# Kernel optimization log

Hardware: AMD Instinct MI355X
Metric: run time of the kernel (lower is better)

## Reference

```python
import jax, jax.numpy as jnp
import numpy as np

T, B, V, L = 512, 32, 512, 128
NEG = -1e9  # safe -inf surrogate (keeps logaddexp gradients finite)


def setup_inputs() -> dict:
    key = jax.random.key(0)
    k1, k2, k3 = jax.random.split(key, 3)
    log_probs = jax.nn.log_softmax(
        jax.random.normal(k1, (T, B, V), dtype=jnp.float32), axis=-1)
    # ASG transition parameter (init ones in the module; use small noise for a
    # non-degenerate reference). transition[i, j] = score of j -> i.
    transition = 0.1 * jax.random.normal(k2, (V, V), dtype=jnp.float32)
    targets = jax.random.randint(k3, (B, L), 0, V)
    input_lengths = jnp.full((B,), T, dtype=jnp.int32)
    target_lengths = jnp.full((B,), L, dtype=jnp.int32)
    return {"log_probs": log_probs, "transition": transition,
            "targets": targets, "input_lengths": input_lengths,
            "target_lengths": target_lengths}


def _fcc(log_probs, transition, input_lengths):
    """Fully-connected criterion: log-partition over all label paths. [B]"""
    def step(alpha, lp_t):  # alpha, lp_t: [B, V]
        # alpha'[b, i] = lp_t[b, i] + logsumexp_j(alpha[b, j] + trans[i, j])
        alpha = lp_t + jax.nn.logsumexp(
            alpha[:, None, :] + transition[None, :, :], axis=2)
        return alpha, jax.nn.logsumexp(alpha, axis=1)

    a0 = log_probs[0]
    _, tail = jax.lax.scan(step, a0, log_probs[1:])
    scores = jnp.concatenate(
        [jax.nn.logsumexp(a0, axis=1)[None], tail], axis=0)  # [T, B]
    return scores[input_lengths - 1, jnp.arange(scores.shape[1])]


def _fac(log_probs, transition, targets, input_lengths, target_lengths):
    """Forced-alignment criterion: DP constrained to the target label seq. [B]"""
    Tt, Bb, _ = log_probs.shape
    Ll = targets.shape[1]
    trans_self = transition[targets, targets]                    # [B, L] stay
    trans_prev = transition[targets[:, 1:], targets[:, :-1]]     # [B, L-1] advance
    # emit[t, b, s] = log_probs[t, b, targets[b, s]]
    emit = jnp.take_along_axis(
        log_probs, jnp.broadcast_to(targets[None], (Tt, Bb, Ll)), axis=2)

    sel = (target_lengths - 1)[:, None]  # [B, 1]

    def final_of(beta):
        return jnp.take_along_axis(beta, sel, axis=1)[:, 0]

    beta0 = jnp.where(jnp.arange(Ll)[None, :] == 0, emit[0], NEG)  # [B, L]

    def step(beta, em_t):
        stay = beta + trans_self
        move = jnp.concatenate(
            [jnp.full((Bb, 1), NEG, beta.dtype),
             beta[:, :-1] + trans_prev], axis=1)
        beta = em_t + jnp.logaddexp(stay, move)
        return beta, final_of(beta)

    _, tail = jax.lax.scan(step, beta0, emit[1:])
    fins = jnp.concatenate([final_of(beta0)[None], tail], axis=0)  # [T, B]
    return fins[input_lengths - 1, jnp.arange(Bb)]


def reference(log_probs, transition, targets, input_lengths, target_lengths):
    # ASG loss (reduction='none'): FCC - FAC, shape [B]
    fcc = _fcc(log_probs, transition, input_lengths)
    fac = _fac(log_probs, transition, targets, input_lengths, target_lengths)
    return fcc - fac
```

## Files before the change

kernel.cpp:

```cpp
#include <hip/hip_runtime.h>
#include <stdint.h>

#define T_ 512
#define B_ 32
#define V_ 512
#define L_ 128
#define NEGF (-1000000000.0f)

#define SE_Q 69.0f
#define SU_Q 127.0f
#define LOGC 9.078313f

typedef int v4i __attribute__((ext_vector_type(4)));

template <int CTRL>
__device__ __forceinline__ int dppmov(int old_, int src) {
    return __builtin_amdgcn_update_dpp(old_, src, CTRL, 0xF, 0xF, false);
}
__device__ __forceinline__ float wave_max64(float x) {
    int xi = __float_as_int(x);
    x = fmaxf(x, __int_as_float(dppmov<0x111>(xi, xi))); xi = __float_as_int(x);
    x = fmaxf(x, __int_as_float(dppmov<0x112>(xi, xi))); xi = __float_as_int(x);
    x = fmaxf(x, __int_as_float(dppmov<0x114>(xi, xi))); xi = __float_as_int(x);
    x = fmaxf(x, __int_as_float(dppmov<0x118>(xi, xi))); xi = __float_as_int(x);
    x = fmaxf(x, __int_as_float(dppmov<0x142>(xi, xi))); xi = __float_as_int(x);
    x = fmaxf(x, __int_as_float(dppmov<0x143>(xi, xi)));
    return x;
}
__device__ __forceinline__ float wave_sum64(float x) {
    int xi = __float_as_int(x);
    x = x + __int_as_float(dppmov<0x111>(xi, xi)); xi = __float_as_int(x);
    x = x + __int_as_float(dppmov<0x112>(xi, xi)); xi = __float_as_int(x);
    x = x + __int_as_float(dppmov<0x114>(xi, xi)); xi = __float_as_int(x);
    x = x + __int_as_float(dppmov<0x118>(xi, xi)); xi = __float_as_int(x);
    x = x + __int_as_float(dppmov<0x142>(xi, xi)); xi = __float_as_int(x);
    x = x + __int_as_float(dppmov<0x143>(xi, xi));
    return x;
}
__device__ __forceinline__ unsigned fkey(float f) {
    unsigned u = __float_as_uint(f);
    return (u & 0x80000000u) ? ~u : (u | 0x80000000u);
}
__device__ __forceinline__ float funkey(unsigned k) {
    unsigned u = (k & 0x80000000u) ? (k ^ 0x80000000u) : ~k;
    return __uint_as_float(u);
}
__device__ __forceinline__ int sel4(v4i a, int r) {
    int x0 = (r & 1) ? a.y : a.x;
    int x1 = (r & 1) ? a.w : a.z;
    return (r & 2) ? x1 : x0;
}

__global__ void asg_prep(const float* __restrict__ trans, uint32_t* __restrict__ Et) {
    int o = blockIdx.x * blockDim.x + threadIdx.x;
    int d    = o & 3;
    int tid  = (o >> 2) & 511;
    int qreg = o >> 11;
    int tt = qreg >> 3, kt = qreg & 7;
    int w = tid >> 6, lane = tid & 63;
    int q = lane >> 4, n = lane & 15;
    int m  = 64 * w + 16 * tt + n;
    int k0 = 64 * kt + 16 * q + 4 * d;
    const float* tp = trans + (size_t)m * V_ + k0;
    uint32_t q0 = (uint32_t)fminf(127.0f, __expf(tp[0]) * SE_Q + 0.5f);
    uint32_t q1 = (uint32_t)fminf(127.0f, __expf(tp[1]) * SE_Q + 0.5f);
    uint32_t q2 = (uint32_t)fminf(127.0f, __expf(tp[2]) * SE_Q + 0.5f);
    uint32_t q3 = (uint32_t)fminf(127.0f, __expf(tp[3]) * SE_Q + 0.5f);
    Et[(size_t)o] = q0 | (q1 << 8) | (q2 << 16) | (q3 << 24);
}

__global__ __attribute__((amdgpu_flat_work_group_size(512, 512),
                          amdgpu_waves_per_eu(2, 2)))
void asg_main(
    const float* __restrict__ lp, const uint32_t* __restrict__ Et,
    const float* __restrict__ trans, const int* __restrict__ targets,
    const int* __restrict__ ilen, const int* __restrict__ tlen,
    float* __restrict__ fcc_ws, float* __restrict__ fac_ws)
{
    __shared__ float facb[256];
    __shared__ __align__(16) uint32_t u_lds[128];
    __shared__ unsigned mslot[2];
    __shared__ unsigned mslotE;
    __shared__ float sumf;

    const int bb  = blockIdx.x;
    const int tid = threadIdx.x;

    if (bb < B_) {
        const int b    = bb;
        const int lane = tid & 63;
        const int w    = tid >> 6;
        const int q    = lane >> 4;
        const int n    = lane & 15;
        const int tt_o = n >> 2;
        const int rg_o = n & 3;
        const int i    = 64 * w + 16 * tt_o + 4 * q + rg_o;
        const int Tlen = ilen[b];

        uint4 er4[32];
        {
            const uint4* Eq = (const uint4*)Et;
            #pragma unroll
            for (int t8 = 0; t8 < 32; ++t8) er4[t8] = Eq[t8 * 512 + tid];
        }

        float alpha = lp[(size_t)b * V_ + i];
        float lpv   = lp[(size_t)1 * (B_ * V_) + (size_t)b * V_ + i];
        if (tid == 511) { mslot[0] = 0u; mslot[1] = 0u; mslotE = 0u; sumf = 0.0f; }
        __syncthreads();

        for (int t = 1; t < Tlen; ++t) {
            {
                float mx = wave_max64(alpha);
                if (lane == 63) atomicMax(&mslot[(t - 1) & 1], fkey(mx));
            }
            __syncthreads();
            float m = funkey(mslot[(t - 1) & 1]);

            {
                float u = __expf(alpha - m);
                uint32_t qu = (uint32_t)(u * SU_Q + 0.5f);
                int pv = (int)(qu << (8 * (i & 3)));
                pv |= dppmov<0xB1>(pv, pv);
                pv |= dppmov<0x4E>(pv, pv);
                if ((i & 3) == 0) u_lds[i >> 2] = (uint32_t)pv;
            }
            if (tid == 511) mslot[t & 1] = 0u;
            __syncthreads();

            int tn = (t + 1 < Tlen) ? (t + 1) : t;
            float lpv_n = lp[(size_t)tn * (B_ * V_) + (size_t)b * V_ + i];

            uint4 bf[8];
            #pragma unroll
            for (int kt = 0; kt < 8; ++kt)
                bf[kt] = *(const uint4*)((const char*)u_lds + 64 * kt + 16 * q);

            v4i a0, a1, a2, a3;
            {
                v4i z = {0, 0, 0, 0};
                a0 = z; a1 = z; a2 = z; a3 = z;
            }
            #pragma unroll
            for (int kt = 0; kt < 8; ++kt) {
                v4i bv = __builtin_bit_cast(v4i, bf[kt]);
                a0 = __builtin_amdgcn_mfma_i32_16x16x64_i8(
                        __builtin_bit_cast(v4i, er4[0 * 8 + kt]), bv, a0, 0, 0, 0);
                a1 = __builtin_amdgcn_mfma_i32_16x16x64_i8(
                        __builtin_bit_cast(v4i, er4[1 * 8 + kt]), bv, a1, 0, 0, 0);
                a2 = __builtin_amdgcn_mfma_i32_16x16x64_i8(
                        __builtin_bit_cast(v4i, er4[2 * 8 + kt]), bv, a2, 0, 0, 0);
                a3 = __builtin_amdgcn_mfma_i32_16x16x64_i8(
                        __builtin_bit_cast(v4i, er4[3 * 8 + kt]), bv, a3, 0, 0, 0);
            }

            int s0 = sel4(a0, rg_o), s1 = sel4(a1, rg_o);
            int s2 = sel4(a2, rg_o), s3 = sel4(a3, rg_o);
            int y0 = (tt_o & 1) ? s1 : s0;
            int y1 = (tt_o & 1) ? s3 : s2;
            int acc = (tt_o & 2) ? y1 : y0;

            alpha = lpv + (m - LOGC) + __logf((float)acc);
            lpv = lpv_n;
        }

        {
            float mx = wave_max64(alpha);
            if (lane == 63) atomicMax(&mslotE, fkey(mx));
        }
        __syncthreads();
        float m2 = funkey(mslotE);
        {
            float sv = wave_sum64(__expf(alpha - m2));
            if (lane == 63) atomicAdd(&sumf, sv);
        }
        __syncthreads();
        if (tid == 0) fcc_ws[b] = m2 + __logf(sumf);
    } else {
        const int b = bb - B_;
        const int l = tid;
        const bool active = (l < L_);
        const int Tlen = ilen[b];
        const int Llen = tlen[b];

        const int tl  = active ? targets[b * L_ + l] : 0;
        const int tlm = (active && l > 0) ? targets[b * L_ + l - 1] : 0;
        const float ts = active ? trans[(size_t)tl * V_ + tl] : 0.0f;
        const float tp = (active && l > 0) ? trans[(size_t)tl * V_ + tlm] : 0.0f;

        float beta = (l == 0) ? lp[(size_t)b * V_ + tl] : NEGF;
        float em_next = active ? lp[(size_t)1 * (B_ * V_) + (size_t)b * V_ + tl] : 0.0f;

        for (int t = 1; t < Tlen; ++t) {
            float* buf = facb + (t & 1) * L_;
            if (active) buf[l] = beta;
            __syncthreads();
            float prev = (active && l > 0) ? buf[l - 1] : NEGF;
            float em = em_next;
            if (active && t + 1 < Tlen)
                em_next = lp[(size_t)(t + 1) * (B_ * V_) + (size_t)b * V_ + tl];
            if (active) {
                float st = beta + ts;
                float mv = prev + tp;
                float mx = fmaxf(st, mv);
                float mn = fminf(st, mv);
                beta = em + mx + log1pf(__expf(mn - mx));
            }
        }
        if (active && l == Llen - 1) fac_ws[b] = beta;
    }
}

__global__ void asg_combine(const float* __restrict__ fcc_ws,
                            const float* __restrict__ fac_ws,
                            float* __restrict__ out) {
    int i = threadIdx.x;
    if (i < B_) out[i] = fcc_ws[i] - fac_ws[i];
}

extern "C" void kernel_launch(void* const* d_in, const int* in_sizes, int n_in,
                              void* d_out, int out_size, void* d_ws, size_t ws_size,
                              hipStream_t stream) {
    const float* lp      = (const float*)d_in[0];
    const float* trans   = (const float*)d_in[1];
    const int*   targets = (const int*)d_in[2];
    const int*   ilen    = (const int*)d_in[3];
    const int*   tlen    = (const int*)d_in[4];
    float* out = (float*)d_out;

    uint32_t* Et     = (uint32_t*)d_ws;
    float*    fcc_ws = (float*)((char*)d_ws + 65536 * 4);
    float*    fac_ws = fcc_ws + B_;

    hipLaunchKernelGGL(asg_prep, dim3(256), dim3(256), 0, stream, trans, Et);
    hipLaunchKernelGGL(asg_main, dim3(2 * B_), dim3(512), 0, stream,
                       lp, Et, trans, targets, ilen, tlen, fcc_ws, fac_ws);
    hipLaunchKernelGGL(asg_combine, dim3(1), dim3(64), 0, stream, fcc_ws, fac_ws, out);
}
```

Baseline: 584.5 us.

## Replace int8 MFMA FCC step with per-thread dot4 and per-wave max scaling

The FCC recurrence no longer uses int8 MFMA tiles. Each thread now owns one output row and computes its row of the quantized transition matvec with v_dot4_i32_i8, with the prep kernel reworked to a plain row-major packed layout. Each wave quantizes exp(alpha) against its own max, read via readlane, instead of a block-wide atomicMax max. Per-wave scale factors are applied as float weights on partial sums. This removes one barrier and the LDS atomics per timestep, and double-buffers LDS, in exchange for far more VALU dot instructions per step than the MFMA path.

```diff
diff --git a/kernel.cpp b/kernel.cpp
--- a/kernel.cpp
+++ b/kernel.cpp
@@ -10,8 +10,6 @@
 #define SE_Q 69.0f
 #define SU_Q 127.0f
 #define LOGC 9.078313f
-
-typedef int v4i __attribute__((ext_vector_type(4)));
 
 template <int CTRL>
 __device__ __forceinline__ int dppmov(int old_, int src) {
@@ -45,27 +43,33 @@
     unsigned u = (k & 0x80000000u) ? (k ^ 0x80000000u) : ~k;
     return __uint_as_float(u);
 }
-__device__ __forceinline__ int sel4(v4i a, int r) {
-    int x0 = (r & 1) ? a.y : a.x;
-    int x1 = (r & 1) ? a.w : a.z;
-    return (r & 2) ? x1 : x0;
+__device__ __forceinline__ int dot4(int a, int b, int c) {
+#if defined(__has_builtin)
+#if __has_builtin(__builtin_amdgcn_sdot4)
+    return __builtin_amdgcn_sdot4(a, b, c, false);
+#else
+    int d;
+    asm("v_dot4_i32_i8 %0, %1, %2, %3" : "=v"(d) : "v"(a), "v"(b), "v"(c));
+    return d;
+#endif
+#else
+    int d;
+    asm("v_dot4_i32_i8 %0, %1, %2, %3" : "=v"(d) : "v"(a), "v"(b), "v"(c));
+    return d;
+#endif
 }
 
 __global__ void asg_prep(const float* __restrict__ trans, uint32_t* __restrict__ Et) {
     int o = blockIdx.x * blockDim.x + threadIdx.x;
-    int d    = o & 3;
-    int tid  = (o >> 2) & 511;
-    int qreg = o >> 11;
-    int tt = qreg >> 3, kt = qreg & 7;
-    int w = tid >> 6, lane = tid & 63;
-    int q = lane >> 4, n = lane & 15;
-    int m  = 64 * w + 16 * tt + n;
-    int k0 = 64 * kt + 16 * q + 4 * d;
-    const float* tp = trans + (size_t)m * V_ + k0;
-    uint32_t q0 = (uint32_t)fminf(127.0f, __expf(tp[0]) * SE_Q + 0.5f);
-    uint32_t q1 = (uint32_t)fminf(127.0f, __expf(tp[1]) * SE_Q + 0.5f);
-    uint32_t q2 = (uint32_t)fminf(127.0f, __expf(tp[2]) * SE_Q + 0.5f);
-    uint32_t q3 = (uint32_t)fminf(127.0f, __expf(tp[3]) * SE_Q + 0.5f);
+    int d = o & 3;
+    int i = (o >> 2) & 511;
+    int j = o >> 11;
+    int k0 = 16 * j + 4 * d;
+    const float4 tv = *(const float4*)(trans + (size_t)i * V_ + k0);
+    uint32_t q0 = (uint32_t)fminf(127.0f, __expf(tv.x) * SE_Q + 0.5f);
+    uint32_t q1 = (uint32_t)fminf(127.0f, __expf(tv.y) * SE_Q + 0.5f);
+    uint32_t q2 = (uint32_t)fminf(127.0f, __expf(tv.z) * SE_Q + 0.5f);
+    uint32_t q3 = (uint32_t)fminf(127.0f, __expf(tv.w) * SE_Q + 0.5f);
     Et[(size_t)o] = q0 | (q1 << 8) | (q2 << 16) | (q3 << 24);
 }
 
@@ -78,8 +82,8 @@
     float* __restrict__ fcc_ws, float* __restrict__ fac_ws)
 {
     __shared__ float facb[256];
-    __shared__ __align__(16) uint32_t u_lds[128];
-    __shared__ unsigned mslot[2];
+    __shared__ __align__(16) uint32_t u_lds[2][128];
+    __shared__ __align__(16) float   mw_lds[2][8];
     __shared__ unsigned mslotE;
     __shared__ float sumf;
 
@@ -90,77 +94,69 @@
         const int b    = bb;
         const int lane = tid & 63;
         const int w    = tid >> 6;
-        const int q    = lane >> 4;
-        const int n    = lane & 15;
-        const int tt_o = n >> 2;
-        const int rg_o = n & 3;
-        const int i    = 64 * w + 16 * tt_o + 4 * q + rg_o;
         const int Tlen = ilen[b];
 
         uint4 er4[32];
         {
             const uint4* Eq = (const uint4*)Et;
             #pragma unroll
-            for (int t8 = 0; t8 < 32; ++t8) er4[t8] = Eq[t8 * 512 + tid];
-        }
-
-        float alpha = lp[(size_t)b * V_ + i];
-        float lpv   = lp[(size_t)1 * (B_ * V_) + (size_t)b * V_ + i];
-        if (tid == 511) { mslot[0] = 0u; mslot[1] = 0u; mslotE = 0u; sumf = 0.0f; }
+            for (int j = 0; j < 32; ++j) er4[j] = Eq[j * 512 + tid];
+        }
+
+        float alpha = lp[(size_t)b * V_ + tid];
+        float lpv   = lp[(size_t)1 * (B_ * V_) + (size_t)b * V_ + tid];
+        if (tid == 0) { mslotE = 0u; sumf = 0.0f; }
         __syncthreads();
 
         for (int t = 1; t < Tlen; ++t) {
+            const int bf = t & 1;
+
+            int tn = (t + 1 < Tlen) ? (t + 1) : t;
+            float lpv_n = lp[(size_t)tn * (B_ * V_) + (size_t)b * V_ + tid];
+
+            float mwp = wave_max64(alpha);
+            float mw  = __int_as_float(
+                __builtin_amdgcn_readlane(__float_as_int(mwp), 63));
+
             {
-                float mx = wave_max64(alpha);
-                if (lane == 63) atomicMax(&mslot[(t - 1) & 1], fkey(mx));
-            }
-            __syncthreads();
-            float m = funkey(mslot[(t - 1) & 1]);
-
-            {
-                float u = __expf(alpha - m);
+                float u = __expf(alpha - mw);
                 uint32_t qu = (uint32_t)(u * SU_Q + 0.5f);
-                int pv = (int)(qu << (8 * (i & 3)));
+                int pv = (int)(qu << (8 * (tid & 3)));
                 pv |= dppmov<0xB1>(pv, pv);
                 pv |= dppmov<0x4E>(pv, pv);
-                if ((i & 3) == 0) u_lds[i >> 2] = (uint32_t)pv;
+                if ((tid & 3) == 0) u_lds[bf][tid >> 2] = (uint32_t)pv;
             }
-            if (tid == 511) mslot[t & 1] = 0u;
+            if (lane == 0) mw_lds[bf][w] = mw;
             __syncthreads();
 
-            int tn = (t + 1 < Tlen) ? (t + 1) : t;
-            float lpv_n = lp[(size_t)tn * (B_ * V_) + (size_t)b * V_ + i];
-
-            uint4 bf[8];
+            float4 m0 = *(const float4*)&mw_lds[bf][0];
+            float4 m1 = *(const float4*)&mw_lds[bf][4];
+            float m = fmaxf(fmaxf(fmaxf(m0.x, m0.y), fmaxf(m0.z, m0.w)),
+                            fmaxf(fmaxf(m1.x, m1.y), fmaxf(m1.z, m1.w)));
+            float sarr[8];
+            sarr[0] = __expf(m0.x - m); sarr[1] = __expf(m0.y - m);
+            sarr[2] = __expf(m0.z - m); sarr[3] = __expf(m0.w - m);
+            sarr[4] = __expf(m1.x - m); sarr[5] = __expf(m1.y - m);
+            sarr[6] = __expf(m1.z - m); sarr[7] = __expf(m1.w - m);
+
+            float accf = 0.0f;
             #pragma unroll
-            for (int kt = 0; kt < 8; ++kt)
-                bf[kt] = *(const uint4*)((const char*)u_lds + 64 * kt + 16 * q);
-
-            v4i a0, a1, a2, a3;
-            {
-                v4i z = {0, 0, 0, 0};
-                a0 = z; a1 = z; a2 = z; a3 = z;
+            for (int c = 0; c < 8; ++c) {
+                const uint4* up = (const uint4*)&u_lds[bf][16 * c];
+                int p0 = 0, p1 = 0;
+                #pragma unroll
+                for (int jj = 0; jj < 4; ++jj) {
+                    uint4 uv = up[jj];
+                    uint4 ev = er4[4 * c + jj];
+                    p0 = dot4((int)ev.x, (int)uv.x, p0);
+                    p1 = dot4((int)ev.y, (int)uv.y, p1);
+                    p0 = dot4((int)ev.z, (int)uv.z, p0);
+                    p1 = dot4((int)ev.w, (int)uv.w, p1);
+                }
+                accf = fmaf(sarr[c], (float)(p0 + p1), accf);
             }
-            #pragma unroll
-            for (int kt = 0; kt < 8; ++kt) {
-                v4i bv = __builtin_bit_cast(v4i, bf[kt]);
-                a0 = __builtin_amdgcn_mfma_i32_16x16x64_i8(
-                        __builtin_bit_cast(v4i, er4[0 * 8 + kt]), bv, a0, 0, 0, 0);
-                a1 = __builtin_amdgcn_mfma_i32_16x16x64_i8(
-                        __builtin_bit_cast(v4i, er4[1 * 8 + kt]), bv, a1, 0, 0, 0);
-                a2 = __builtin_amdgcn_mfma_i32_16x16x64_i8(
-                        __builtin_bit_cast(v4i, er4[2 * 8 + kt]), bv, a2, 0, 0, 0);
-                a3 = __builtin_amdgcn_mfma_i32_16x16x64_i8(
-                        __builtin_bit_cast(v4i, er4[3 * 8 + kt]), bv, a3, 0, 0, 0);
-            }
-
-            int s0 = sel4(a0, rg_o), s1 = sel4(a1, rg_o);
-            int s2 = sel4(a2, rg_o), s3 = sel4(a3, rg_o);
-            int y0 = (tt_o & 1) ? s1 : s0;
-            int y1 = (tt_o & 1) ? s3 : s2;
-            int acc = (tt_o & 2) ? y1 : y0;
-
-            alpha = lpv + (m - LOGC) + __logf((float)acc);
+
+            alpha = lpv + (m - LOGC) + __logf(accf);
             lpv = lpv_n;
         }
 
```

Measured after the change: 711.8 us. 1.22x slower.

## Process two batch rows per FCC block in linear-domain scaled recurrence

Applied to the files above, without the earlier changes.

Each FCC block now handles two batch elements, running two independent int8 MFMA recurrences per step so one chain's reductions and barriers overlap with the other's matrix work. The recurrence keeps alpha in the linear domain (exp(lp) times the previous integer accumulator) with a running log-scale sum. This removes the per-step exp/log of alpha, and the per-step max now uses per-wave LDS slots with a float4 read instead of atomics. It halves the FCC block count and amortizes the barriers across two rows, but each step does twice the serial MFMA work per block and the quantization scaling changes numerically.

```diff
diff --git a/kernel.cpp b/kernel.cpp
--- a/kernel.cpp
+++ b/kernel.cpp
@@ -78,16 +78,19 @@
     float* __restrict__ fcc_ws, float* __restrict__ fac_ws)
 {
     __shared__ float facb[256];
-    __shared__ __align__(16) uint32_t u_lds[128];
-    __shared__ unsigned mslot[2];
-    __shared__ unsigned mslotE;
-    __shared__ float sumf;
+    __shared__ __align__(16) uint32_t uA_lds[128];
+    __shared__ __align__(16) uint32_t uB_lds[128];
+    __shared__ __align__(16) float mwA[8];
+    __shared__ __align__(16) float mwB[8];
+    __shared__ unsigned mslotA, mslotB;
+    __shared__ float sumfA, sumfB;
 
     const int bb  = blockIdx.x;
     const int tid = threadIdx.x;
 
-    if (bb < B_) {
-        const int b    = bb;
+    if (bb < B_ / 2) {
+        const int bA   = 2 * bb;
+        const int bB   = 2 * bb + 1;
         const int lane = tid & 63;
         const int w    = tid >> 6;
         const int q    = lane >> 4;
@@ -95,7 +98,9 @@
         const int tt_o = n >> 2;
         const int rg_o = n & 3;
         const int i    = 64 * w + 16 * tt_o + 4 * q + rg_o;
-        const int Tlen = ilen[b];
+        const int TlenA = ilen[bA];
+        const int TlenB = ilen[bB];
+        const int Tmax  = (TlenA > TlenB) ? TlenA : TlenB;
 
         uint4 er4[32];
         {
@@ -104,80 +109,161 @@
             for (int t8 = 0; t8 < 32; ++t8) er4[t8] = Eq[t8 * 512 + tid];
         }
 
-        float alpha = lp[(size_t)b * V_ + i];
-        float lpv   = lp[(size_t)1 * (B_ * V_) + (size_t)b * V_ + i];
-        if (tid == 511) { mslot[0] = 0u; mslot[1] = 0u; mslotE = 0u; sumf = 0.0f; }
+        float lpv0A = lp[(size_t)bA * V_ + i];
+        float lpv0B = lp[(size_t)bB * V_ + i];
+        float elpA = __expf(lpv0A), elpB = __expf(lpv0B);
+        float lpvA = lp[(size_t)(B_ * V_) + (size_t)bA * V_ + i];
+        float lpvB = lp[(size_t)(B_ * V_) + (size_t)bB * V_ + i];
+        float accfA = 1.0f, accfB = 1.0f;
+        float SA = 0.0f, SB = 0.0f;
+        if (tid == 0) { mslotA = 0u; mslotB = 0u; sumfA = 0.0f; sumfB = 0.0f; }
         __syncthreads();
 
-        for (int t = 1; t < Tlen; ++t) {
-            {
-                float mx = wave_max64(alpha);
-                if (lane == 63) atomicMax(&mslot[(t - 1) & 1], fkey(mx));
-            }
+        for (int t = 1; t < Tmax; ++t) {
+            float keyA = elpA * accfA;
+            float keyB = elpB * accfB;
+            float mxA = wave_max64(keyA);
+            float mxB = wave_max64(keyB);
+            if (lane == 63) { mwA[w] = mxA; mwB[w] = mxB; }
             __syncthreads();
-            float m = funkey(mslot[(t - 1) & 1]);
-
-            {
-                float u = __expf(alpha - m);
-                uint32_t qu = (uint32_t)(u * SU_Q + 0.5f);
+
+            float4 a0 = *(const float4*)&mwA[0];
+            float4 a1 = *(const float4*)&mwA[4];
+            float4 b0 = *(const float4*)&mwB[0];
+            float4 b1 = *(const float4*)&mwB[4];
+            float kmA = fmaxf(fmaxf(fmaxf(a0.x, a0.y), fmaxf(a0.z, a0.w)),
+                              fmaxf(fmaxf(a1.x, a1.y), fmaxf(a1.z, a1.w)));
+            float kmB = fmaxf(fmaxf(fmaxf(b0.x, b0.y), fmaxf(b0.z, b0.w)),
+                              fmaxf(fmaxf(b1.x, b1.y), fmaxf(b1.z, b1.w)));
+            float rA = 127.0f * __builtin_amdgcn_rcpf(kmA);
+            float rB = 127.0f * __builtin_amdgcn_rcpf(kmB);
+            {
+                uint32_t qu = (uint32_t)fminf(127.0f, fmaf(keyA, rA, 0.5f));
                 int pv = (int)(qu << (8 * (i & 3)));
                 pv |= dppmov<0xB1>(pv, pv);
                 pv |= dppmov<0x4E>(pv, pv);
-                if ((i & 3) == 0) u_lds[i >> 2] = (uint32_t)pv;
-            }
-            if (tid == 511) mslot[t & 1] = 0u;
+                if ((i & 3) == 0) uA_lds[i >> 2] = (uint32_t)pv;
+            }
+            {
+                uint32_t qu = (uint32_t)fminf(127.0f, fmaf(keyB, rB, 0.5f));
+                int pv = (int)(qu << (8 * (i & 3)));
+                pv |= dppmov<0xB1>(pv, pv);
+                pv |= dppmov<0x4E>(pv, pv);
+                if ((i & 3) == 0) uB_lds[i >> 2] = (uint32_t)pv;
+            }
             __syncthreads();
 
-            int tn = (t + 1 < Tlen) ? (t + 1) : t;
-            float lpv_n = lp[(size_t)tn * (B_ * V_) + (size_t)b * V_ + i];
-
-            uint4 bf[8];
+            uint4 bfA[8];
             #pragma unroll
             for (int kt = 0; kt < 8; ++kt)
-                bf[kt] = *(const uint4*)((const char*)u_lds + 64 * kt + 16 * q);
-
-            v4i a0, a1, a2, a3;
+                bfA[kt] = *(const uint4*)((const char*)uA_lds + 64 * kt + 16 * q);
+
+            int tnA = (t + 1 < TlenA) ? (t + 1) : (TlenA - 1);
+            float lpvA_n = lp[(size_t)tnA * (B_ * V_) + (size_t)bA * V_ + i];
+            float elpA_n = __expf(lpvA);
+
+            v4i c0, c1, c2, c3;
             {
                 v4i z = {0, 0, 0, 0};
-                a0 = z; a1 = z; a2 = z; a3 = z;
+                c0 = z; c1 = z; c2 = z; c3 = z;
             }
             #pragma unroll
             for (int kt = 0; kt < 8; ++kt) {
-                v4i bv = __builtin_bit_cast(v4i, bf[kt]);
-                a0 = __builtin_amdgcn_mfma_i32_16x16x64_i8(
-                        __builtin_bit_cast(v4i, er4[0 * 8 + kt]), bv, a0, 0, 0, 0);
-                a1 = __builtin_amdgcn_mfma_i32_16x16x64_i8(
-                        __builtin_bit_cast(v4i, er4[1 * 8 + kt]), bv, a1, 0, 0, 0);
-                a2 = __builtin_amdgcn_mfma_i32_16x16x64_i8(
-                        __builtin_bit_cast(v4i, er4[2 * 8 + kt]), bv, a2, 0, 0, 0);
-                a3 = __builtin_amdgcn_mfma_i32_16x16x64_i8(
-                        __builtin_bit_cast(v4i, er4[3 * 8 + kt]), bv, a3, 0, 0, 0);
-            }
-
-            int s0 = sel4(a0, rg_o), s1 = sel4(a1, rg_o);
-            int s2 = sel4(a2, rg_o), s3 = sel4(a3, rg_o);
-            int y0 = (tt_o & 1) ? s1 : s0;
-            int y1 = (tt_o & 1) ? s3 : s2;
-            int acc = (tt_o & 2) ? y1 : y0;
-
-            alpha = lpv + (m - LOGC) + __logf((float)acc);
-            lpv = lpv_n;
-        }
-
+                v4i bv = __builtin_bit_cast(v4i, bfA[kt]);
+                c0 = __builtin_amdgcn_mfma_i32_16x16x64_i8(
+                        __builtin_bit_cast(v4i, er4[0 * 8 + kt]), bv, c0, 0, 0, 0);
+                c1 = __builtin_amdgcn_mfma_i32_16x16x64_i8(
+                        __builtin_bit_cast(v4i, er4[1 * 8 + kt]), bv, c1, 0, 0, 0);
+                c2 = __builtin_amdgcn_mfma_i32_16x16x64_i8(
+                        __builtin_bit_cast(v4i, er4[2 * 8 + kt]), bv, c2, 0, 0, 0);
+                c3 = __builtin_amdgcn_mfma_i32_16x16x64_i8(
+                        __builtin_bit_cast(v4i, er4[3 * 8 + kt]), bv, c3, 0, 0, 0);
+            }
+            int accA;
+            {
+                int s0 = sel4(c0, rg_o), s1 = sel4(c1, rg_o);
+                int s2 = sel4(c2, rg_o), s3 = sel4(c3, rg_o);
+                int y0 = (tt_o & 1) ? s1 : s0;
+                int y1 = (tt_o & 1) ? s3 : s2;
+                accA = (tt_o & 2) ? y1 : y0;
+            }
+
+            uint4 bfB[8];
+            #pragma unroll
+            for (int kt = 0; kt < 8; ++kt)
+                bfB[kt] = *(const uint4*)((const char*)uB_lds + 64 * kt + 16 * q);
+
+            int tnB = (t + 1 < TlenB) ? (t + 1) : (TlenB - 1);
+            float lpvB_n = lp[(size_t)tnB * (B_ * V_) + (size_t)bB * V_ + i];
+            float elpB_n = __expf(lpvB);
+
+            {
+                v4i z = {0, 0, 0, 0};
+                c0 = z; c1 = z; c2 = z; c3 = z;
+            }
+            #pragma unroll
+            for (int kt = 0; kt < 8; ++kt) {
+                v4i bv = __builtin_bit_cast(v4i, bfB[kt]);
+                c0 = __builtin_amdgcn_mfma_i32_16x16x64_i8(
+                        __builtin_bit_cast(v4i, er4[0 * 8 + kt]), bv, c0, 0, 0, 0);
+                c1 = __builtin_amdgcn_mfma_i32_16x16x64_i8(
+                        __builtin_bit_cast(v4i, er4[1 * 8 + kt]), bv, c1, 0, 0, 0);
+                c2 = __builtin_amdgcn_mfma_i32_16x16x64_i8(
+                        __builtin_bit_cast(v4i, er4[2 * 8 + kt]), bv, c2, 0, 0, 0);
+                c3 = __builtin_amdgcn_mfma_i32_16x16x64_i8(
+                        __builtin_bit_cast(v4i, er4[3 * 8 + kt]), bv, c3, 0, 0, 0);
+            }
+            int accB;
+            {
+                int s0 = sel4(c0, rg_o), s1 = sel4(c1, rg_o);
+                int s2 = sel4(c2, rg_o), s3 = sel4(c3, rg_o);
+                int y0 = (tt_o & 1) ? s1 : s0;
+                int y1 = (tt_o & 1) ? s3 : s2;
+                accB = (tt_o & 2) ? y1 : y0;
+            }
+
+            if (t < TlenA) {
+                accfA = (float)accA;
+                SA += __logf(kmA) - LOGC;
+                elpA = elpA_n;
+                lpvA = lpvA_n;
+            }
+            if (t < TlenB) {
+                accfB = (float)accB;
+                SB += __logf(kmB) - LOGC;
+                elpB = elpB_n;
+                lpvB = lpvB_n;
+            }
+        }
+
+        float alphaA = ((TlenA > 1) ? lpvA : lpv0A) + SA + __logf(accfA);
+        float alphaB = ((TlenB > 1) ? lpvB : lpv0B) + SB + __logf(accfB);
         {
-            float mx = wave_max64(alpha);
-            if (lane == 63) atomicMax(&mslotE, fkey(mx));
+            float mA = wave_max64(alphaA);
+            float mB = wave_max64(alphaB);
+            if (lane == 63) {
+                atomicMax(&mslotA, fkey(mA));
+                atomicMax(&mslotB, fkey(mB));
+            }
         }
         __syncthreads();
-        float m2 = funkey(mslotE);
+        float m2A = funkey(mslotA);
+        float m2B = funkey(mslotB);
         {
-            float sv = wave_sum64(__expf(alpha - m2));
-            if (lane == 63) atomicAdd(&sumf, sv);
+            float svA = wave_sum64(__expf(alphaA - m2A));
+            float svB = wave_sum64(__expf(alphaB - m2B));
+            if (lane == 63) {
+                atomicAdd(&sumfA, svA);
+                atomicAdd(&sumfB, svB);
+            }
         }
         __syncthreads();
-        if (tid == 0) fcc_ws[b] = m2 + __logf(sumf);
+        if (tid == 0) {
+            fcc_ws[bA] = m2A + __logf(sumfA);
+            fcc_ws[bB] = m2B + __logf(sumfB);
+        }
     } else {
-        const int b = bb - B_;
+        const int b = bb - B_ / 2;
         const int l = tid;
         const bool active = (l < L_);
         const int Tlen = ilen[b];
@@ -233,7 +319,7 @@
     float*    fac_ws = fcc_ws + B_;
 
     hipLaunchKernelGGL(asg_prep, dim3(256), dim3(256), 0, stream, trans, Et);
-    hipLaunchKernelGGL(asg_main, dim3(2 * B_), dim3(512), 0, stream,
+    hipLaunchKernelGGL(asg_main, dim3(B_ / 2 + B_), dim3(512), 0, stream,
                        lp, Et, trans, targets, ilen, tlen, fcc_ws, fac_ws);
     hipLaunchKernelGGL(asg_combine, dim3(1), dim3(64), 0, stream, fcc_ws, fac_ws, out);
 }
```

Result: slower. 938.3 us (+60.5%).
